# Kernel tuning notes

Measured on AMD Instinct MI355X. Metric: run time of the kernel, lower is better.

The kernel has to match this reference:

```python
import jax, jax.numpy as jnp
import numpy as np

T = 4096          # num tokens
HID = 2048        # hidden_size
HQ = 32           # num q heads
HKV = 8           # num kv heads
G = HQ // HKV     # GQA group size
D = 128           # head_dim (q/k)
DV = 96           # v_head_dim
W = 512           # sliding window (= query block size)
THETA = 1e6
Q_SIZE, K_SIZE, V_SIZE = HQ * D, HKV * D, HKV * DV


def setup_inputs() -> dict:
    key = jax.random.key(0)
    k1, k2, k3, k4 = jax.random.split(key, 4)
    positions = jnp.arange(T, dtype=jnp.int32)
    hidden_states = jax.random.normal(k1, (T, HID), dtype=jnp.float32)
    qkv_w = jax.random.normal(k2, (Q_SIZE + K_SIZE + V_SIZE, HID), dtype=jnp.float32) * (HID ** -0.5)
    o_w = jax.random.normal(k3, (HID, HQ * DV), dtype=jnp.float32) * ((HQ * DV) ** -0.5)
    sink_bias = jax.random.normal(k4, (HQ,), dtype=jnp.float32)
    return {"positions": positions, "hidden_states": hidden_states,
            "qkv_w": qkv_w, "o_w": o_w, "sink_bias": sink_bias}


def _rope(x, positions):
    # neox-style rotate-half RoPE on full head_dim (partial_rotary_factor=1.0)
    half = D // 2
    inv_freq = 1.0 / (THETA ** (jnp.arange(0, half, dtype=jnp.float32) / half))
    ang = positions.astype(jnp.float32)[:, None] * inv_freq[None, :]   # [T, D/2]
    cos = jnp.cos(ang)[:, None, :]
    sin = jnp.sin(ang)[:, None, :]
    x1, x2 = x[..., :half], x[..., half:]
    return jnp.concatenate([x1 * cos - x2 * sin, x2 * cos + x1 * sin], axis=-1)


def _swa_with_sink(q, k, v, sink_bias):
    # q: [T, HKV, G, D], k: [T, HKV, D], v: [T, HKV, DV]
    nb = T // W
    scale = D ** -0.5
    qb = q.reshape(nb, W, HKV, G, D)
    # per query block i, keys/values from global span [(i-1)*W, (i+1)*W)
    k_pad = jnp.pad(k, ((W, 0), (0, 0), (0, 0)))
    v_pad = jnp.pad(v, ((W, 0), (0, 0), (0, 0)))
    idx = jnp.arange(nb)[:, None] * W + jnp.arange(2 * W)[None, :]     # [nb, 2W]
    k_ext = k_pad[idx]                                                 # [nb, 2W, HKV, D]
    v_ext = v_pad[idx]                                                 # [nb, 2W, HKV, DV]
    # mask: rel = t - j in [0, W); exclude left-pad keys (key_pos < 0)
    r = jnp.arange(W)[:, None]
    c = jnp.arange(2 * W)[None, :]
    rel = W + r - c                                                    # [W, 2W]
    key_pos = (jnp.arange(nb)[:, None, None] - 1) * W + c[None]        # [nb, W(1), 2W]
    mask = (rel >= 0) & (rel < W) & (key_pos >= 0)                     # [nb, W, 2W]
    scores = jnp.einsum('nrkgd,nckd->nkgrc', qb, k_ext) * scale        # [nb,HKV,G,W,2W]
    scores = jnp.where(mask[:, None, None, :, :], scores, -jnp.inf)
    sink = jnp.broadcast_to(sink_bias.reshape(HKV, G)[None, :, :, None, None],
                            (nb, HKV, G, W, 1))
    logits = jnp.concatenate([scores, sink], axis=-1)                  # [...,2W+1]
    p = jax.nn.softmax(logits, axis=-1)[..., :-1]                      # drop sink column
    out = jnp.einsum('nkgrc,nckd->nrkgd', p, v_ext)                    # [nb,W,HKV,G,DV]
    return out.reshape(T, HQ * DV)


def reference(positions, hidden_states, qkv_w, o_w, sink_bias):
    qkv = hidden_states @ qkv_w.T                                      # [T, Q+K+V]
    q, k, v = jnp.split(qkv, [Q_SIZE, Q_SIZE + K_SIZE], axis=-1)
    q = q.reshape(T, HQ, D)
    k = k.reshape(T, HKV, D)
    v = v.reshape(T, HKV, DV)
    q = _rope(q, positions).reshape(T, HKV, G, D)
    k = _rope(k, positions)
    attn = _swa_with_sink(q, k, v, sink_bias)                          # [T, HQ*DV]
    return attn @ o_w.T                                                # [T, HID]
```

## Files before the change

### kernel.cpp

```cpp
#include <hip/hip_runtime.h>
#include <hip/hip_bf16.h>
#include <stdint.h>

#define T_SEQ 4096
#define HIDDEN 2048
#define NQH 32
#define NKVH 8
#define DH 128
#define DVH 96
#define WWIN 512
#define QKVN 5888
#define KOFF 4096
#define VOFF 5120
#define ATTN 3072
#define QSCALE 0.08838834764831845f

typedef uint16_t u16;
typedef uint32_t u32;
typedef __bf16 bfrag8 __attribute__((ext_vector_type(8)));
typedef float f32x4v __attribute__((ext_vector_type(4)));
typedef float f32x16 __attribute__((ext_vector_type(16)));

__device__ __forceinline__ u16 f2bf(float x) {
  u32 u = __float_as_uint(x);
  return (u16)((u + 0x7fffu + ((u >> 16) & 1u)) >> 16);
}
__device__ __forceinline__ float bf2f(u16 v) { return __uint_as_float(((u32)v) << 16); }

__device__ __forceinline__ void gload16(const u16* src, char* ldst) {
  __builtin_amdgcn_global_load_lds((const __attribute__((address_space(1))) u32*)src,
                                   (__attribute__((address_space(3))) u32*)ldst, 16, 0, 0);
}

__global__ void cvt3_kernel(const float* __restrict__ i1, const float* __restrict__ i2,
                            const float* __restrict__ i3,
                            u16* __restrict__ o1, u16* __restrict__ o2, u16* __restrict__ o3,
                            int n1, int n2, int n3) {
  int i = blockIdx.x * blockDim.x + threadIdx.x;
  int st = gridDim.x * blockDim.x;
  int total = n1 + n2 + n3;
  for (; i < total; i += st) {
    const float4* src;
    ushort4* dst;
    int j;
    if (i < n1) { src = (const float4*)i1; dst = (ushort4*)o1; j = i; }
    else if (i < n1 + n2) { src = (const float4*)i2; dst = (ushort4*)o2; j = i - n1; }
    else { src = (const float4*)i3; dst = (ushort4*)o3; j = i - n1 - n2; }
    float4 v = src[j];
    ushort4 o;
    o.x = f2bf(v.x); o.y = f2bf(v.y); o.z = f2bf(v.z); o.w = f2bf(v.w);
    dst[j] = o;
  }
}

template<int OUT_F32>
__global__ __launch_bounds__(512, 4) void gemm_v3k32(const u16* __restrict__ A,
                                                     const u16* __restrict__ B,
                                                     void* __restrict__ Cp,
                                                     int M, int N, int K, int nbm) {
  extern __shared__ char lds[];
  const int tid = threadIdx.x;
  const int w = tid >> 6, lane = tid & 63;
  const int wr = w >> 1, wc = w & 1;
  const int r5 = lane & 31, kg = lane >> 5;

  const int nwg = gridDim.x;
  int bid = (int)blockIdx.x;
  if ((nwg & 7) == 0) bid = (bid & 7) * (nwg >> 3) + (bid >> 3);
  const int bm = (bid % nbm) * 256;
  const int bn = (bid / nbm) * 128;
  const int NT = K >> 5;

  f32x16 acc[2][2];
#pragma unroll
  for (int mb = 0; mb < 2; mb++)
#pragma unroll
    for (int nb = 0; nb < 2; nb++)
#pragma unroll
      for (int i = 0; i < 16; i++) acc[mb][nb][i] = 0.f;

  const int q = r5 * 64 + ((kg ^ (r5 & 3)) << 4);

  auto stage = [&](int t) {
    char* dst = lds + (t % 3) * 24576;
    const u16* Abase = A + (size_t)bm * K + ((size_t)t << 5);
    const u16* Bbase = B + (size_t)bn * K + ((size_t)t << 5);
#pragma unroll
    for (int i = 0; i < 2; i++) {
      int D = (i * 512 + tid) * 16;
      int row = D >> 6;
      int kb = (D ^ ((row & 3) << 4)) & 63;
      gload16(Abase + (size_t)row * K + (kb >> 1), dst + D);
    }
    {
      int D = tid * 16;
      int row = D >> 6;
      int kb = (D ^ ((row & 3) << 4)) & 63;
      gload16(Bbase + (size_t)row * K + (kb >> 1), dst + 16384 + D);
    }
  };

  stage(0);

  for (int t = 0; t < NT; ++t) {
    const char* Ab = lds + (t % 3) * 24576 + wr * 4096;
    const char* Bb = lds + (t % 3) * 24576 + 16384 + wc * 4096;
    if (t + 1 < NT) {
      stage(t + 1);
      asm volatile("s_waitcnt vmcnt(3)");
    } else {
      asm volatile("s_waitcnt vmcnt(0)");
    }
    asm volatile("s_barrier" ::: "memory");

    bfrag8 af[2][2], bf[2][2];
#pragma unroll
    for (int ks = 0; ks < 2; ks++) {
#pragma unroll
      for (int mb = 0; mb < 2; mb++)
        af[mb][ks] = *(const bfrag8*)(Ab + mb * 2048 + (q ^ (ks << 5)));
#pragma unroll
      for (int nb = 0; nb < 2; nb++)
        bf[nb][ks] = *(const bfrag8*)(Bb + nb * 2048 + (q ^ (ks << 5)));
    }
    __builtin_amdgcn_s_setprio(1);
#pragma unroll
    for (int ks = 0; ks < 2; ks++)
#pragma unroll
      for (int mb = 0; mb < 2; mb++)
#pragma unroll
        for (int nb = 0; nb < 2; nb++)
          acc[mb][nb] = __builtin_amdgcn_mfma_f32_32x32x16_bf16(af[mb][ks], bf[nb][ks], acc[mb][nb], 0, 0, 0);
    __builtin_amdgcn_s_setprio(0);
  }

  const int rb0 = bm + wr * 64;
  const int cb0 = bn + wc * 64;
#pragma unroll
  for (int mb = 0; mb < 2; mb++)
#pragma unroll
    for (int nb = 0; nb < 2; nb++)
#pragma unroll
      for (int i = 0; i < 16; i++) {
        int rowl = (i & 3) + 8 * (i >> 2) + 4 * kg;
        size_t off = (size_t)(rb0 + mb * 32 + rowl) * N + cb0 + nb * 32 + r5;
        if (OUT_F32) ((float*)Cp)[off] = acc[mb][nb][i];
        else         ((u16*)Cp)[off] = f2bf(acc[mb][nb][i]);
      }
}

template<int OUT_F32>
__global__ __launch_bounds__(512, 2) void gemm_v3(const u16* __restrict__ A,
                                                  const u16* __restrict__ B,
                                                  void* __restrict__ Cp,
                                                  int M, int N, int K, int nbm) {
  extern __shared__ char lds[];
  const int tid = threadIdx.x;
  const int w = tid >> 6, lane = tid & 63;
  const int wr = w >> 1, wc = w & 1;
  const int r5 = lane & 31, kg = lane >> 5;

  const int nwg = gridDim.x;
  int bid = (int)blockIdx.x;
  if ((nwg & 7) == 0) bid = (bid & 7) * (nwg >> 3) + (bid >> 3);
  const int bm = (bid % nbm) * 256;
  const int bn = (bid / nbm) * 128;
  const int NT = K >> 6;

  f32x16 acc[2][2];
#pragma unroll
  for (int mb = 0; mb < 2; mb++)
#pragma unroll
    for (int nb = 0; nb < 2; nb++)
#pragma unroll
      for (int i = 0; i < 16; i++) acc[mb][nb][i] = 0.f;

  const int q = r5 * 128 + ((kg ^ (r5 & 7)) << 4);

  auto stageA = [&](int t) {
    char* dst = lds + (t % 3) * 49152;
    const u16* Abase = A + (size_t)bm * K + ((size_t)t << 6);
#pragma unroll
    for (int i = 0; i < 4; i++) {
      int D = (w * 4 + i) * 1024 + lane * 16;
      int row = D >> 7;
      int kb = (D ^ ((row & 7) << 4)) & 127;
      gload16(Abase + (size_t)row * K + (kb >> 1), dst + D);
    }
  };
  auto stageB = [&](int t) {
    char* dst = lds + (t % 3) * 49152 + 32768;
    const u16* Bbase = B + (size_t)bn * K + ((size_t)t << 6);
#pragma unroll
    for (int i = 0; i < 2; i++) {
      int D = (w * 2 + i) * 1024 + lane * 16;
      int row = D >> 7;
      int kb = (D ^ ((row & 7) << 4)) & 127;
      gload16(Bbase + (size_t)row * K + (kb >> 1), dst + D);
    }
  };

  stageA(0); stageB(0);

  for (int t = 0; t < NT; ++t) {
    const char* Ab = lds + (t % 3) * 49152 + wr * 8192;
    const char* Bb = lds + (t % 3) * 49152 + 32768 + wc * 8192;
    if (t + 1 < NT) {
      stageA(t + 1);
      stageB(t + 1);
      asm volatile("s_waitcnt vmcnt(6)");
    } else {
      asm volatile("s_waitcnt vmcnt(0)");
    }
    asm volatile("s_barrier" ::: "memory");

    bfrag8 af[2][2], bf[2][2];
#pragma unroll
    for (int ks = 0; ks < 2; ks++) {
#pragma unroll
      for (int mb = 0; mb < 2; mb++)
        af[mb][ks] = *(const bfrag8*)(Ab + mb * 4096 + (q ^ (ks << 5)));
#pragma unroll
      for (int nb = 0; nb < 2; nb++)
        bf[nb][ks] = *(const bfrag8*)(Bb + nb * 4096 + (q ^ (ks << 5)));
    }
    __builtin_amdgcn_s_setprio(1);
#pragma unroll
    for (int ks = 0; ks < 2; ks++)
#pragma unroll
      for (int mb = 0; mb < 2; mb++)
#pragma unroll
        for (int nb = 0; nb < 2; nb++)
          acc[mb][nb] = __builtin_amdgcn_mfma_f32_32x32x16_bf16(af[mb][ks], bf[nb][ks], acc[mb][nb], 0, 0, 0);
    __builtin_amdgcn_s_setprio(0);

    bfrag8 af2[2][2], bf2[2][2];
#pragma unroll
    for (int ks = 0; ks < 2; ks++) {
#pragma unroll
      for (int mb = 0; mb < 2; mb++)
        af2[mb][ks] = *(const bfrag8*)(Ab + mb * 4096 + (q ^ ((ks + 2) << 5)));
#pragma unroll
      for (int nb = 0; nb < 2; nb++)
        bf2[nb][ks] = *(const bfrag8*)(Bb + nb * 4096 + (q ^ ((ks + 2) << 5)));
    }
    __builtin_amdgcn_s_setprio(1);
#pragma unroll
    for (int ks = 0; ks < 2; ks++)
#pragma unroll
      for (int mb = 0; mb < 2; mb++)
#pragma unroll
        for (int nb = 0; nb < 2; nb++)
          acc[mb][nb] = __builtin_amdgcn_mfma_f32_32x32x16_bf16(af2[mb][ks], bf2[nb][ks], acc[mb][nb], 0, 0, 0);
    __builtin_amdgcn_s_setprio(0);
  }

  const int rb0 = bm + wr * 64;
  const int cb0 = bn + wc * 64;
#pragma unroll
  for (int mb = 0; mb < 2; mb++)
#pragma unroll
    for (int nb = 0; nb < 2; nb++)
#pragma unroll
      for (int i = 0; i < 16; i++) {
        int rowl = (i & 3) + 8 * (i >> 2) + 4 * kg;
        size_t off = (size_t)(rb0 + mb * 32 + rowl) * N + cb0 + nb * 32 + r5;
        if (OUT_F32) ((float*)Cp)[off] = acc[mb][nb][i];
        else         ((u16*)Cp)[off] = f2bf(acc[mb][nb][i]);
      }
}

template<int OUT_F32>
__global__ __launch_bounds__(256) void gemm_nt(const u16* __restrict__ A,
                                               const u16* __restrict__ B,
                                               void* __restrict__ Cp,
                                               int M, int N, int K) {
  __shared__ u16 Asm[128 * 32];
  __shared__ u16 Bsm[128 * 32];
  const int tid = threadIdx.x;
  const int wv = tid >> 6, lane = tid & 63;
  const int bm = blockIdx.x * 128, bn = blockIdx.y * 128;
  const int wm = (wv >> 1) * 64, wn = (wv & 1) * 64;
  const int srow = lane >> 2;
  const int scol = (lane & 3) * 8;
  const int fr = lane & 15, fk = (lane >> 4) * 8;
  f32x4v acc[4][4];
#pragma unroll
  for (int i = 0; i < 4; i++)
#pragma unroll
    for (int j = 0; j < 4; j++) acc[i][j] = {0.f, 0.f, 0.f, 0.f};

  for (int kt = 0; kt < K; kt += 32) {
    __syncthreads();
#pragma unroll
    for (int c = 0; c < 2; c++) {
      const int ci = wv * 2 + c;
      const u16* ga = A + (size_t)(bm + ci * 16 + srow) * K + kt + scol;
      const u16* gb = B + (size_t)(bn + ci * 16 + srow) * K + kt + scol;
      gload16(ga, (char*)(Asm + ci * 512));
      gload16(gb, (char*)(Bsm + ci * 512));
    }
    __syncthreads();
    bfrag8 af[4], bf[4];
#pragma unroll
    for (int i = 0; i < 4; i++) af[i] = *(const bfrag8*)(Asm + (wm + i * 16 + fr) * 32 + fk);
#pragma unroll
    for (int j = 0; j < 4; j++) bf[j] = *(const bfrag8*)(Bsm + (wn + j * 16 + fr) * 32 + fk);
#pragma unroll
    for (int i = 0; i < 4; i++)
#pragma unroll
      for (int j = 0; j < 4; j++)
        acc[i][j] = __builtin_amdgcn_mfma_f32_16x16x32_bf16(af[i], bf[j], acc[i][j], 0, 0, 0);
  }
  const int orow = (lane >> 4) * 4, ocol = lane & 15;
#pragma unroll
  for (int i = 0; i < 4; i++)
#pragma unroll
    for (int j = 0; j < 4; j++) {
      size_t base = (size_t)(bm + wm + i * 16 + orow) * N + (size_t)(bn + wn + j * 16 + ocol);
#pragma unroll
      for (int r = 0; r < 4; r++) {
        if (OUT_F32) ((float*)Cp)[base + (size_t)r * N] = acc[i][j][r];
        else         ((u16*)Cp)[base + (size_t)r * N] = f2bf(acc[i][j][r]);
      }
    }
}

__global__ void rope_kernel(u16* __restrict__ qkv, const int* __restrict__ pos) {
  int gid = blockIdx.x * 256 + threadIdx.x;
  int dc = gid & 7;
  int r = gid >> 3;
  int hh = r % 40;
  int t = r / 40;
  if (t >= T_SEQ) return;
  int off = (hh < 32) ? hh * 128 : KOFF + (hh - 32) * 128;
  u16* p = qkv + (size_t)t * QKVN + off + dc * 8;
  uint4 a = *(const uint4*)p;
  uint4 b = *(const uint4*)(p + 64);
  const u32* aw = (const u32*)&a;
  const u32* bw = (const u32*)&b;
  float pt = (float)pos[t];
  float sc = (hh < 32) ? QSCALE : 1.0f;
  union { uint4 v; u16 s[8]; } ra, rb;
#pragma unroll
  for (int j = 0; j < 8; j++) {
    int d = dc * 8 + j;
    float inv_freq = exp2f(-(float)d * 0.3114307588956852f);
    float ang = pt * inv_freq;
    float cs = cosf(ang), sn = sinf(ang);
    float x1 = bf2f((u16)(aw[j >> 1] >> ((j & 1) * 16)));
    float x2 = bf2f((u16)(bw[j >> 1] >> ((j & 1) * 16)));
    ra.s[j] = f2bf((x1 * cs - x2 * sn) * sc);
    rb.s[j] = f2bf((x2 * cs + x1 * sn) * sc);
  }
  *(uint4*)p = ra.v;
  *(uint4*)(p + 64) = rb.v;
}

__global__ __launch_bounds__(256) void vt_kernel(const u16* __restrict__ qkv,
                                                 u16* __restrict__ vt) {
  __shared__ u16 tile[64][100];
  const int t0 = blockIdx.x * 64;
  const int hk = blockIdx.y;
  const int tid = threadIdx.x;
#pragma unroll
  for (int i = 0; i < 3; i++) {
    int idx = i * 256 + tid;
    int row = idx / 12, ch = idx % 12;
    const u16* g = qkv + (size_t)(t0 + row) * QKVN + VOFF + hk * DVH + ch * 8;
    uint2 a = *(const uint2*)g;
    uint2 b = *(const uint2*)(g + 4);
    *(uint2*)&tile[row][ch * 8] = a;
    *(uint2*)&tile[row][ch * 8 + 4] = b;
  }
  __syncthreads();
#pragma unroll
  for (int i = 0; i < 3; i++) {
    int idx = i * 256 + tid;
    int dv = idx >> 3, tc = (idx & 7) * 8;
    union { uint4 v4; u16 s[8]; } o;
#pragma unroll
    for (int j = 0; j < 8; j++) o.s[j] = tile[tc + j][dv];
    *(uint4*)(vt + (((size_t)(hk * 96 + dv)) << 12) + t0 + tc) = o.v4;
  }
}

__global__ __launch_bounds__(256, 2) void attn_mfma(const u16* __restrict__ qkv,
                                                    const u16* __restrict__ vt,
                                                    const float* __restrict__ sink_bias,
                                                    u16* __restrict__ attn_out) {
  extern __shared__ char smem[];

  const int tid = threadIdx.x;
  const int wv = tid >> 6;
  const int lane = tid & 63;
  const int g = lane >> 4;
  const int c = lane & 15;
  const int t0 = blockIdx.x * 32;
  const int hk = blockIdx.y;
  const int h = hk * 4 + wv;
  u16* pw = (u16*)(smem + 57344 + wv * 4096);

  bfrag8 qf[2][4];
#pragma unroll
  for (int m = 0; m < 2; m++)
#pragma unroll
    for (int kf = 0; kf < 4; kf++)
      qf[m][kf] = *(const bfrag8*)(qkv + (size_t)(t0 + m * 16 + c) * QKVN + h * DH + kf * 32 + g * 8);

  f32x4v acc_o[2][6];
#pragma unroll
  for (int m = 0; m < 2; m++)
#pragma unroll
    for (int n = 0; n < 6; n++) acc_o[m][n] = {0.f, 0.f, 0.f, 0.f};

  const float sb = sink_bias[h];
  float m_run[2][4], l_run[2][4];
#pragma unroll
  for (int m = 0; m < 2; m++)
#pragma unroll
    for (int r = 0; r < 4; r++) { m_run[m][r] = sb; l_run[m][r] = 1.0f; }

  int cb0 = t0 - (WWIN - 1);
  cb0 = (cb0 < 0) ? 0 : (cb0 & ~63);
  const int nc = (t0 + 32 - cb0 + 63) >> 6;

  auto stage = [&](int ci) {
    const int cb = cb0 + ci * 64;
    char* kd = smem + (ci & 1) * 16384;
    char* vd = smem + 32768 + (ci & 1) * 12288;
#pragma unroll
    for (int it = 0; it < 4; it++) {
      int dest = it * 4096 + tid * 16;
      int row = dest >> 8;
      int src = dest ^ ((row & 7) << 4);
      gload16(qkv + (size_t)(cb + row) * QKVN + KOFF + hk * DH + ((src & 255) >> 1), kd + dest);
    }
#pragma unroll
    for (int it = 0; it < 3; it++) {
      int dest = it * 4096 + tid * 16;
      int row = dest >> 7;
      int src = dest ^ ((row & 7) << 4);
      gload16(vt + (((size_t)(hk * 96 + row)) << 12) + cb + ((src & 127) >> 1), vd + dest);
    }
  };

  stage(0);
  if (nc > 1) stage(1);

  for (int ci = 0; ci < nc; ci++) {
    const int cb = cb0 + ci * 64;
    const char* k_lds = smem + (ci & 1) * 16384;
    const char* v_lds = smem + 32768 + (ci & 1) * 12288;
    if (ci + 1 < nc) asm volatile("s_waitcnt vmcnt(7)");
    else             asm volatile("s_waitcnt vmcnt(0)");
    asm volatile("s_barrier" ::: "memory");

    f32x4v s[2][4];
#pragma unroll
    for (int m = 0; m < 2; m++)
#pragma unroll
      for (int n = 0; n < 4; n++) s[m][n] = {0.f, 0.f, 0.f, 0.f};
#pragma unroll
    for (int kf = 0; kf < 4; kf++) {
      bfrag8 kb[4];
#pragma unroll
      for (int n = 0; n < 4; n++) {
        int key = n * 16 + c;
        int byt = ((key << 8) + (kf << 6) + (g << 4)) ^ ((key & 7) << 4);
        kb[n] = *(const bfrag8*)(k_lds + byt);
      }
#pragma unroll
      for (int m = 0; m < 2; m++)
#pragma unroll
        for (int n = 0; n < 4; n++)
          s[m][n] = __builtin_amdgcn_mfma_f32_16x16x32_bf16(qf[m][kf], kb[n], s[m][n], 0, 0, 0);
    }

    if ((cb + 63 > t0) || (cb + WWIN < t0 + 32)) {
#pragma unroll
      for (int m = 0; m < 2; m++)
#pragma unroll
        for (int n = 0; n < 4; n++)
#pragma unroll
          for (int r = 0; r < 4; r++) {
            int rel = (t0 + m * 16 + g * 4 + r) - (cb + n * 16 + c);
            if (!(rel >= 0 && rel < WWIN)) s[m][n][r] = -3.0e38f;
          }
    }

    float corr[2][4];
    bool grew = false;
#pragma unroll
    for (int m = 0; m < 2; m++)
#pragma unroll
      for (int r = 0; r < 4; r++) {
        float v0 = fmaxf(fmaxf(s[m][0][r], s[m][1][r]), fmaxf(s[m][2][r], s[m][3][r]));
        v0 = fmaxf(v0, __shfl_xor(v0, 1));
        v0 = fmaxf(v0, __shfl_xor(v0, 2));
        v0 = fmaxf(v0, __shfl_xor(v0, 4));
        v0 = fmaxf(v0, __shfl_xor(v0, 8));
        float mo = m_run[m][r];
        float mn = fmaxf(mo, v0);
        corr[m][r] = __expf(mo - mn);
        grew |= (mn > mo);
        m_run[m][r] = mn;
        float p0 = __expf(s[m][0][r] - mn);
        float p1 = __expf(s[m][1][r] - mn);
        float p2 = __expf(s[m][2][r] - mn);
        float p3 = __expf(s[m][3][r] - mn);
        s[m][0][r] = p0; s[m][1][r] = p1; s[m][2][r] = p2; s[m][3][r] = p3;
        float rs = p0 + p1 + p2 + p3;
        rs += __shfl_xor(rs, 1);
        rs += __shfl_xor(rs, 2);
        rs += __shfl_xor(rs, 4);
        rs += __shfl_xor(rs, 8);
        l_run[m][r] = l_run[m][r] * corr[m][r] + rs;
      }
    if (__any(grew)) {
#pragma unroll
      for (int m = 0; m < 2; m++)
#pragma unroll
        for (int n = 0; n < 6; n++)
#pragma unroll
        for (int r = 0; r < 4; r++) acc_o[m][n][r] *= corr[m][r];
    }

#pragma unroll
    for (int m = 0; m < 2; m++)
#pragma unroll
      for (int n = 0; n < 4; n++) {
        u32 lo = (u32)f2bf(s[m][n][0]) | ((u32)f2bf(s[m][n][1]) << 16);
        u32 hi = (u32)f2bf(s[m][n][2]) | ((u32)f2bf(s[m][n][3]) << 16);
        int byt = ((m * 2 + (n >> 1)) << 10) | (g << 3) | ((c & 3) << 5) |
                  (((c >> 2) & 1) << 9) | ((((n & 1) * 2) + (c >> 3)) << 7);
        uint2 u; u.x = lo; u.y = hi;
        *(uint2*)((char*)pw + byt) = u;
      }

#pragma unroll
    for (int ks = 0; ks < 2; ks++) {
      bfrag8 pa[2];
#pragma unroll
      for (int m = 0; m < 2; m++) {
        union { bfrag8 v; u16 s16[8]; } u;
#pragma unroll
        for (int j = 0; j < 4; j++) {
          int e = ((m * 2 + ks) << 9) + c + j * 16 + g * 64;
          u.s16[j] = pw[e];
          u.s16[4 + j] = pw[e + 256];
        }
        pa[m] = u.v;
      }
#pragma unroll
      for (int n = 0; n < 6; n++) {
        int dv = n * 16 + c;
        int byt = ((dv << 7) + (ks << 6) + (g << 4)) ^ ((dv & 7) << 4);
        bfrag8 vb = *(const bfrag8*)(v_lds + byt);
#pragma unroll
        for (int m = 0; m < 2; m++)
          acc_o[m][n] = __builtin_amdgcn_mfma_f32_16x16x32_bf16(pa[m], vb, acc_o[m][n], 0, 0, 0);
      }
    }

    asm volatile("s_barrier" ::: "memory");
    if (ci + 2 < nc) stage(ci + 2);
  }

#pragma unroll
  for (int m = 0; m < 2; m++) {
    float inv[4];
#pragma unroll
    for (int r = 0; r < 4; r++) inv[r] = 1.0f / l_run[m][r];
#pragma unroll
    for (int n = 0; n < 6; n++)
#pragma unroll
      for (int r = 0; r < 4; r++) {
        int tq = t0 + m * 16 + g * 4 + r;
        attn_out[(size_t)tq * ATTN + h * DVH + n * 16 + c] = f2bf(acc_o[m][n][r] * inv[r]);
      }
  }
}

extern "C" void kernel_launch(void* const* d_in, const int* in_sizes, int n_in,
                              void* d_out, int out_size, void* d_ws, size_t ws_size,
                              hipStream_t stream) {
  const int* positions = (const int*)d_in[0];
  const float* hidden = (const float*)d_in[1];
  const float* qkv_w = (const float*)d_in[2];
  const float* o_w = (const float*)d_in[3];
  const float* sink = (const float*)d_in[4];
  char* ws = (char*)d_ws;

  u16* hs_bf   = (u16*)(ws + 0);
  u16* w1_bf   = (u16*)(ws + 16777216);
  u16* attn_bf = (u16*)(ws + 0);
  u16* vt_buf  = (u16*)(ws + 25165824);
  u16* w2_bf   = (u16*)(ws + 40894464);
  u16* qkv_bf  = (u16*)(ws + 53477376);

  bool k32Ok = (hipFuncSetAttribute((const void*)&gemm_v3k32<0>,
                  hipFuncAttributeMaxDynamicSharedMemorySize, 73728) == hipSuccess);
  bool v3Ok = (hipFuncSetAttribute((const void*)&gemm_v3<1>,
                  hipFuncAttributeMaxDynamicSharedMemorySize, 147456) == hipSuccess);
  (void)hipFuncSetAttribute((const void*)&attn_mfma,
                            hipFuncAttributeMaxDynamicSharedMemorySize, 73728);

  cvt3_kernel<<<dim3(2048), dim3(256), 0, stream>>>(hidden, qkv_w, o_w,
                                                    hs_bf, w1_bf, w2_bf,
                                                    2097152, 3014656, 1572864);

  if (k32Ok)
    gemm_v3k32<0><<<dim3(736), dim3(512), 73728, stream>>>(hs_bf, w1_bf, (void*)qkv_bf,
                                                           T_SEQ, QKVN, HIDDEN, 16);
  else
    gemm_nt<0><<<dim3(32, 46), dim3(256), 0, stream>>>(hs_bf, w1_bf, (void*)qkv_bf,
                                                       T_SEQ, QKVN, HIDDEN);

  rope_kernel<<<dim3(5120), dim3(256), 0, stream>>>(qkv_bf, positions);
  vt_kernel<<<dim3(T_SEQ / 64, NKVH), dim3(256), 0, stream>>>(qkv_bf, vt_buf);
  attn_mfma<<<dim3(T_SEQ / 32, NKVH), dim3(256), 73728, stream>>>(qkv_bf, vt_buf, sink, attn_bf);

  if (v3Ok)
    gemm_v3<1><<<dim3(256), dim3(512), 147456, stream>>>(attn_bf, w2_bf, d_out,
                                                         T_SEQ, HIDDEN, ATTN, 16);
  else
    gemm_nt<1><<<dim3(32, 16), dim3(256), 0, stream>>>(attn_bf, w2_bf, d_out,
                                                       T_SEQ, HIDDEN, ATTN);
}
```

Before: 321.3 us.

## Rewrite QKV GEMM with 4 waves, 128x64 per-wave tiles using 16x16x32 MFMA

The QKV projection GEMM drops from 8 waves to 4 per 256x128 block, so each wave now computes a 128x64 sub-tile with 8x4 accumulators of 16x16x32 bf16 MFMA instead of 2x2 32x32x16 fragments. The LDS layout and swizzle are changed to match the 16x16 fragment loads, and each thread now issues more global loads per stage, with the waitcnt raised to match. The aim is more register-level reuse per LDS read and fewer waves contending for LDS. The cost is lower occupancy, higher register pressure, and more load instructions per thread.

```diff
diff --git a/kernel.cpp b/kernel.cpp
--- a/kernel.cpp
+++ b/kernel.cpp
@@ -54,15 +54,15 @@
 }
 
 template<int OUT_F32>
-__global__ __launch_bounds__(512, 4) void gemm_v3k32(const u16* __restrict__ A,
-                                                     const u16* __restrict__ B,
-                                                     void* __restrict__ Cp,
-                                                     int M, int N, int K, int nbm) {
+__global__ __launch_bounds__(256, 2) void gemm_v5(const u16* __restrict__ A,
+                                                  const u16* __restrict__ B,
+                                                  void* __restrict__ Cp,
+                                                  int M, int N, int K, int nbm) {
   extern __shared__ char lds[];
   const int tid = threadIdx.x;
   const int w = tid >> 6, lane = tid & 63;
   const int wr = w >> 1, wc = w & 1;
-  const int r5 = lane & 31, kg = lane >> 5;
+  const int fr = lane & 15, kg = lane >> 4;
 
   const int nwg = gridDim.x;
   int bid = (int)blockIdx.x;
@@ -71,82 +71,83 @@
   const int bn = (bid / nbm) * 128;
   const int NT = K >> 5;
 
-  f32x16 acc[2][2];
-#pragma unroll
-  for (int mb = 0; mb < 2; mb++)
-#pragma unroll
-    for (int nb = 0; nb < 2; nb++)
-#pragma unroll
-      for (int i = 0; i < 16; i++) acc[mb][nb][i] = 0.f;
-
-  const int q = r5 * 64 + ((kg ^ (r5 & 3)) << 4);
+  f32x4v acc[8][4];
+#pragma unroll
+  for (int mf = 0; mf < 8; mf++)
+#pragma unroll
+    for (int nf = 0; nf < 4; nf++) acc[mf][nf] = {0.f, 0.f, 0.f, 0.f};
 
   auto stage = [&](int t) {
     char* dst = lds + (t % 3) * 24576;
     const u16* Abase = A + (size_t)bm * K + ((size_t)t << 5);
     const u16* Bbase = B + (size_t)bn * K + ((size_t)t << 5);
 #pragma unroll
+    for (int i = 0; i < 8; i++) {
+      int D = (i * 256 + tid) * 16;
+      int L = D ^ (((D >> 7) & 7) << 4);
+      int m = ((D >> 7) << 1) | ((L >> 6) & 1);
+      int k = (L & 63) >> 1;
+      gload16(Abase + (size_t)m * K + k, dst + D);
+    }
+#pragma unroll
     for (int i = 0; i < 2; i++) {
-      int D = (i * 512 + tid) * 16;
-      int row = D >> 6;
-      int kb = (D ^ ((row & 3) << 4)) & 63;
-      gload16(Abase + (size_t)row * K + (kb >> 1), dst + D);
-    }
-    {
-      int D = tid * 16;
-      int row = D >> 6;
-      int kb = (D ^ ((row & 3) << 4)) & 63;
-      gload16(Bbase + (size_t)row * K + (kb >> 1), dst + 16384 + D);
+      int D = (i * 256 + tid) * 16;
+      int L = D ^ (((D >> 7) & 7) << 4);
+      int mcol = ((D >> 7) << 1) | ((L >> 6) & 1);
+      int k = (L & 63) >> 1;
+      gload16(Bbase + (size_t)mcol * K + k, dst + 16384 + D);
     }
   };
 
   stage(0);
 
   for (int t = 0; t < NT; ++t) {
-    const char* Ab = lds + (t % 3) * 24576 + wr * 4096;
+    const char* Ab = lds + (t % 3) * 24576 + wr * 8192;
     const char* Bb = lds + (t % 3) * 24576 + 16384 + wc * 4096;
     if (t + 1 < NT) {
       stage(t + 1);
-      asm volatile("s_waitcnt vmcnt(3)");
+      asm volatile("s_waitcnt vmcnt(10)");
     } else {
       asm volatile("s_waitcnt vmcnt(0)");
     }
     asm volatile("s_barrier" ::: "memory");
 
-    bfrag8 af[2][2], bf[2][2];
-#pragma unroll
-    for (int ks = 0; ks < 2; ks++) {
-#pragma unroll
-      for (int mb = 0; mb < 2; mb++)
-        af[mb][ks] = *(const bfrag8*)(Ab + mb * 2048 + (q ^ (ks << 5)));
-#pragma unroll
-      for (int nb = 0; nb < 2; nb++)
-        bf[nb][ks] = *(const bfrag8*)(Bb + nb * 2048 + (q ^ (ks << 5)));
+    bfrag8 bf[4];
+#pragma unroll
+    for (int nf = 0; nf < 4; nf++) {
+      int c2 = nf * 16 + fr;
+      int byt = (((c2 >> 1) << 7) | ((c2 & 1) << 6) | (kg << 4)) ^ (((c2 >> 1) & 7) << 4);
+      bf[nf] = *(const bfrag8*)(Bb + byt);
+    }
+    bfrag8 af[8];
+#pragma unroll
+    for (int mf = 0; mf < 8; mf++) {
+      int r2 = mf * 16 + fr;
+      int byt = (((r2 >> 1) << 7) | ((r2 & 1) << 6) | (kg << 4)) ^ (((r2 >> 1) & 7) << 4);
+      af[mf] = *(const bfrag8*)(Ab + byt);
     }
     __builtin_amdgcn_s_setprio(1);
 #pragma unroll
-    for (int ks = 0; ks < 2; ks++)
-#pragma unroll
-      for (int mb = 0; mb < 2; mb++)
-#pragma unroll
-        for (int nb = 0; nb < 2; nb++)
-          acc[mb][nb] = __builtin_amdgcn_mfma_f32_32x32x16_bf16(af[mb][ks], bf[nb][ks], acc[mb][nb], 0, 0, 0);
+    for (int mf = 0; mf < 8; mf++)
+#pragma unroll
+      for (int nf = 0; nf < 4; nf++)
+        acc[mf][nf] = __builtin_amdgcn_mfma_f32_16x16x32_bf16(af[mf], bf[nf], acc[mf][nf], 0, 0, 0);
     __builtin_amdgcn_s_setprio(0);
   }
 
-  const int rb0 = bm + wr * 64;
+  const int rb0 = bm + wr * 128;
   const int cb0 = bn + wc * 64;
 #pragma unroll
-  for (int mb = 0; mb < 2; mb++)
-#pragma unroll
-    for (int nb = 0; nb < 2; nb++)
-#pragma unroll
-      for (int i = 0; i < 16; i++) {
-        int rowl = (i & 3) + 8 * (i >> 2) + 4 * kg;
-        size_t off = (size_t)(rb0 + mb * 32 + rowl) * N + cb0 + nb * 32 + r5;
-        if (OUT_F32) ((float*)Cp)[off] = acc[mb][nb][i];
-        else         ((u16*)Cp)[off] = f2bf(acc[mb][nb][i]);
-      }
+  for (int mf = 0; mf < 8; mf++)
+#pragma unroll
+    for (int nf = 0; nf < 4; nf++) {
+      size_t base = (size_t)(rb0 + mf * 16 + kg * 4) * N + cb0 + nf * 16 + fr;
+#pragma unroll
+      for (int r = 0; r < 4; r++) {
+        if (OUT_F32) ((float*)Cp)[base + (size_t)r * N] = acc[mf][nf][r];
+        else         ((u16*)Cp)[base + (size_t)r * N] = f2bf(acc[mf][nf][r]);
+      }
+    }
 }
 
 template<int OUT_F32>
@@ -599,7 +600,7 @@
   u16* w2_bf   = (u16*)(ws + 40894464);
   u16* qkv_bf  = (u16*)(ws + 53477376);
 
-  bool k32Ok = (hipFuncSetAttribute((const void*)&gemm_v3k32<0>,
+  bool v5Ok = (hipFuncSetAttribute((const void*)&gemm_v5<0>,
                   hipFuncAttributeMaxDynamicSharedMemorySize, 73728) == hipSuccess);
   bool v3Ok = (hipFuncSetAttribute((const void*)&gemm_v3<1>,
                   hipFuncAttributeMaxDynamicSharedMemorySize, 147456) == hipSuccess);
@@ -610,9 +611,9 @@
                                                     hs_bf, w1_bf, w2_bf,
                                                     2097152, 3014656, 1572864);
 
-  if (k32Ok)
-    gemm_v3k32<0><<<dim3(736), dim3(512), 73728, stream>>>(hs_bf, w1_bf, (void*)qkv_bf,
-                                                           T_SEQ, QKVN, HIDDEN, 16);
+  if (v5Ok)
+    gemm_v5<0><<<dim3(736), dim3(256), 73728, stream>>>(hs_bf, w1_bf, (void*)qkv_bf,
+                                                        T_SEQ, QKVN, HIDDEN, 16);
   else
     gemm_nt<0><<<dim3(32, 46), dim3(256), 0, stream>>>(hs_bf, w1_bf, (void*)qkv_bf,
                                                        T_SEQ, QKVN, HIDDEN);
```

After: 335.8 us. +4.5%, slower.
